# Optimization experiments

Hardware: AMD Instinct MI355X
Metric: run time of the kernel (lower is better)

The kernel has to match this reference:

```python
import jax, jax.numpy as jnp
import numpy as np

EPS = 1e-5
K = 3
K2 = K * K


def _conv(x, w, pad=0):
    return jax.lax.conv_general_dilated(
        x, w, (1, 1), [(pad, pad), (pad, pad)],
        dimension_numbers=('NCHW', 'OIHW', 'NCHW'))


def _bn_silu(x, gamma, beta, mean, var):
    scale = (gamma / jnp.sqrt(var + EPS))[None, :, None, None]
    y = (x - mean[None, :, None, None]) * scale + beta[None, :, None, None]
    return y * jax.nn.sigmoid(y)  # SiLU


def _space_to_depth(x, s=2):
    b, c, h, w = x.shape
    x = x.reshape(b, c, h // s, s, w // s, s)
    x = x.transpose(0, 1, 3, 5, 2, 4)
    return x.reshape(b, c * s * s, h // s, w // s)


def _deform_sample(x, offset, mask, pad=1):
    # x: (B,C,H,W); offset: (B,2*K2,H,W) layout [kk -> (dy,dx)]; mask: (B,K2,H,W)
    B, C, H, W = x.shape
    off = offset.reshape(B, K2, 2, H, W)
    oy, ox = off[:, :, 0], off[:, :, 1]
    ki = jnp.repeat(jnp.arange(K), K)  # kernel row (y), (K2,)
    kj = jnp.tile(jnp.arange(K), K)    # kernel col (x), (K2,)
    base_y = (jnp.arange(H)[None, :, None] - pad + ki[:, None, None]).astype(x.dtype)  # (K2,H,1)
    base_x = (jnp.arange(W)[None, None, :] - pad + kj[:, None, None]).astype(x.dtype)  # (K2,1,W)
    py = base_y[None] + oy  # (B,K2,H,W)
    px = base_x[None] + ox

    y0 = jnp.floor(py)
    x0 = jnp.floor(px)
    wy = py - y0
    wx = px - x0
    y0i = y0.astype(jnp.int32)
    x0i = x0.astype(jnp.int32)

    xf = x.reshape(B, C, H * W)
    gather = jax.vmap(lambda a, i: a[:, i])  # (C,HW),(N)->(C,N)

    out = jnp.zeros((B, C, K2, H, W), x.dtype)
    for dy in (0, 1):
        for dx in (0, 1):
            yi = y0i + dy
            xi = x0i + dx
            valid = (yi >= 0) & (yi < H) & (xi >= 0) & (xi < W)
            w = (wy if dy else 1.0 - wy) * (wx if dx else 1.0 - wx) * valid
            idx = (jnp.clip(yi, 0, H - 1) * W + jnp.clip(xi, 0, W - 1)).reshape(B, -1)
            vals = gather(xf, idx).reshape(B, C, K2, H, W)
            out = out + vals * w[:, None]
    return out * mask[:, None]  # modulated


def setup_inputs() -> dict:
    key = jax.random.key(0)
    ks = jax.random.split(key, 12)
    B, C1, H, W = 8, 128, 160, 160
    C_SPD, C_MID, C2 = C1 * 4, 128, 256
    inp = {
        'x': jax.random.normal(ks[0], (B, C1, H, W), jnp.float32),
        'reduce_w': jax.random.normal(ks[1], (C_MID, C_SPD, 1, 1), jnp.float32) * 0.05,
        'reduce_gamma': jax.random.uniform(ks[2], (C_MID,), jnp.float32, 0.5, 1.5),
        'reduce_beta': jax.random.normal(ks[3], (C_MID,), jnp.float32) * 0.1,
        'reduce_mean': jax.random.normal(ks[4], (C_MID,), jnp.float32) * 0.1,
        'reduce_var': jax.random.uniform(ks[5], (C_MID,), jnp.float32, 0.5, 1.5),
        'off_w': jax.random.normal(ks[6], (27, C_MID, 3, 3), jnp.float32) * 0.01,
        'off_b': jnp.zeros((27,), jnp.float32),
        'dcn_w': jax.random.normal(ks[7], (C2, C_MID, 3, 3), jnp.float32) * 0.03,
        'dcn_gamma': jax.random.uniform(ks[8], (C2,), jnp.float32, 0.5, 1.5),
        'dcn_beta': jax.random.normal(ks[9], (C2,), jnp.float32) * 0.1,
        'dcn_mean': jax.random.normal(ks[10], (C2,), jnp.float32) * 0.1,
        'dcn_var': jax.random.uniform(ks[11], (C2,), jnp.float32, 0.5, 1.5),
    }
    return inp


def reference(x, reduce_w, reduce_gamma, reduce_beta, reduce_mean, reduce_var,
              off_w, off_b, dcn_w, dcn_gamma, dcn_beta, dcn_mean, dcn_var):
    # SPD: (B,C,H,W) -> (B,4C,H/2,W/2)
    x = _space_to_depth(x, 2)
    # 1x1 reduce + BN + SiLU
    x = _bn_silu(_conv(x, reduce_w), reduce_gamma, reduce_beta, reduce_mean, reduce_var)
    # offset/mask prediction (3x3 conv, pad=1)
    om = _conv(x, off_w, pad=1) + off_b[None, :, None, None]
    offset = om[:, :2 * K2]
    mask = jax.nn.sigmoid(om[:, 2 * K2:3 * K2])
    # modulated deformable 3x3 conv (stride 1, pad 1)
    samp = _deform_sample(x, offset, mask, pad=1)  # (B,C_mid,9,H,W)
    O = dcn_w.shape[0]
    out = jnp.einsum('bckhw,ock->bohw', samp, dcn_w.reshape(O, dcn_w.shape[1], K2))
    return _bn_silu(out, dcn_gamma, dcn_beta, dcn_mean, dcn_var)
```

## Files before the change

### kernel.cpp

```cpp
#include <hip/hip_runtime.h>

constexpr int HW  = 6400;
constexpr int WW  = 80;

typedef __attribute__((ext_vector_type(8))) short short8;
typedef __attribute__((ext_vector_type(4))) float f32x4;
typedef unsigned short ushort_t;

__device__ __forceinline__ float sigmoidf_(float x) { return 1.f / (1.f + __expf(-x)); }
__device__ __forceinline__ float siluf_(float y) { return y / (1.f + __expf(-y)); }
__device__ __forceinline__ ushort_t f2bf(float f) {
    unsigned u = __float_as_uint(f);
    u += 0x7FFFu + ((u >> 16) & 1u);
    return (ushort_t)(u >> 16);
}
__device__ __forceinline__ float bf2f(ushort_t h) {
    return __uint_as_float(((unsigned)h) << 16);
}
__device__ __forceinline__ int xcd_bid800(int b) { return (b & 7) * 100 + (b >> 3); }

__global__ __launch_bounds__(256) void k0_prep(
    const float* __restrict__ rw, const float* __restrict__ ow,
    const float* __restrict__ dw,
    const float* __restrict__ rg, const float* __restrict__ rb,
    const float* __restrict__ rm, const float* __restrict__ rv,
    ushort_t* __restrict__ WB,
    ushort_t* __restrict__ WoB, ushort_t* __restrict__ WdB,
    float* __restrict__ scr, float* __restrict__ shr)
{
    const int i = blockIdx.x * 256 + threadIdx.x;
    if (blockIdx.x == 0 && threadIdx.x < 128) {
        const int m = threadIdx.x;
        const float sc = rg[m] * rsqrtf(rv[m] + 1e-5f);
        scr[m] = sc;
        shr[m] = rb[m] - rm[m] * sc;
    }
    if (i < 65536) {
        const int e = i & 7;
        const int lane = (i >> 3) & 63;
        const int chunkW = i >> 9;
        const int nt = chunkW >> 4, kks = chunkW & 15;
        const int kk = kks * 32 + ((lane >> 4) << 3) + e;
        const int o = (nt << 4) + (lane & 15);
        WB[i] = f2bf(rw[o * 512 + kk]);
    }
    const int j = i - 65536;
    if (j >= 0 && j < 36864) {
        const int e = j & 7;
        const int lane = (j >> 3) & 63;
        const int chunk = j >> 9;
        const int nf = chunk / 36, ksg = chunk % 36;
        const int kk = ksg * 32 + ((lane >> 4) << 3) + e;
        const int q = kk >> 7, c = kk & 127;
        const int o = (nf << 4) + (lane & 15);
        WoB[j] = (o < 27) ? f2bf(ow[o * 1152 + c * 9 + q]) : (ushort_t)0;
    }
    const int l = j - 36864;
    if (l >= 0 && l < 294912) {
        const int e = l & 7;
        const int lane = (l >> 3) & 63;
        const int chunk = l >> 9;
        const int ot = chunk / 36, ksg = chunk % 36;
        const int kk = ksg * 32 + ((lane >> 4) << 3) + e;
        const int tap = kk >> 7, c = kk & 127;
        const int o = (ot << 4) + (lane & 15);
        WdB[l] = f2bf(dw[o * 1152 + c * 9 + tap]);
    }
}

__global__ __launch_bounds__(256) void k1_reduce(
    const float* __restrict__ x,
    const ushort_t* __restrict__ WB,
    const float* __restrict__ scr, const float* __restrict__ shr,
    ushort_t* __restrict__ xm_bf)
{
    const int t    = threadIdx.x;
    const int lane = t & 63;
    const int wave = t >> 6;
    const int q = lane >> 4, ln = lane & 15;
    const int p0 = xcd_bid800(blockIdx.x) * 64;
    const int bb = p0 / HW;
    const int px = wave * 16 + ln;
    const int hw = (p0 % HW) + px;
    const int h = hw / WW, w = hw % WW;
    const float* xb = x + (size_t)bb * 128 * 25600 + (2 * h) * 160 + 2 * w;

    f32x4 acc[8] = {};

#pragma unroll 4
    for (int kks = 0; kks < 16; ++kks) {
        const int c0 = kks * 8 + q * 2;
        const float* pc0 = xb + (size_t)c0 * 25600;
        const float* pc1 = pc0 + 25600;
        const float2 a0 = *reinterpret_cast<const float2*>(pc0);
        const float2 a1 = *reinterpret_cast<const float2*>(pc0 + 160);
        const float2 b0 = *reinterpret_cast<const float2*>(pc1);
        const float2 b1 = *reinterpret_cast<const float2*>(pc1 + 160);
        short8 p;
        p[0] = (short)f2bf(a0.x); p[1] = (short)f2bf(a0.y);
        p[2] = (short)f2bf(a1.x); p[3] = (short)f2bf(a1.y);
        p[4] = (short)f2bf(b0.x); p[5] = (short)f2bf(b0.y);
        p[6] = (short)f2bf(b1.x); p[7] = (short)f2bf(b1.y);
#pragma unroll
        for (int nt = 0; nt < 8; ++nt) {
            const short8 wf = *reinterpret_cast<const short8*>(WB + ((nt << 4) + kks) * 512 + lane * 8);
            acc[nt] = __builtin_amdgcn_mfma_f32_16x16x32_bf16(wf, p, acc[nt], 0, 0, 0);
        }
    }

    const int pi = p0 + px;
    ushort_t* op = xm_bf + (size_t)pi * 128;
#pragma unroll
    for (int nt = 0; nt < 8; ++nt) {
        const int ob = nt * 16 + q * 4;
        const float4 s4 = *reinterpret_cast<const float4*>(scr + ob);
        const float4 b4 = *reinterpret_cast<const float4*>(shr + ob);
        const float y0 = siluf_(acc[nt][0] * s4.x + b4.x);
        const float y1 = siluf_(acc[nt][1] * s4.y + b4.y);
        const float y2 = siluf_(acc[nt][2] * s4.z + b4.z);
        const float y3 = siluf_(acc[nt][3] * s4.w + b4.w);
        *reinterpret_cast<uint2*>(op + ob) =
            make_uint2(f2bf(y0) | ((unsigned)f2bf(y1) << 16),
                       f2bf(y2) | ((unsigned)f2bf(y3) << 16));
    }
}

__global__ __launch_bounds__(256) void k2_off(
    const ushort_t* __restrict__ xm_bf, const ushort_t* __restrict__ WoB,
    const float* __restrict__ obias, float* __restrict__ om)
{
    __shared__ __align__(16) ushort_t A[2][64 * 128];
    __shared__ __align__(16) float T[32 * 64];

    const int t = threadIdx.x;
    const int lane = t & 63;
    const int wave = t >> 6;
    const int p0 = xcd_bid800(blockIdx.x) * 64;
    const int bb = p0 / HW;
    const int hw0 = p0 % HW;

    const int spx = t & 63;
    const int hws = hw0 + spx;
    const int hh = hws / WW, wwp = hws % WW;

    auto STAGE = [&](int q, int buf) {
        const int dy = q / 3 - 1, dx = q % 3 - 1;
        const int y = hh + dy, xx = wwp + dx;
        const bool valid = ((unsigned)y < 80u) && ((unsigned)xx < 80u);
        const ushort_t* src = xm_bf + ((size_t)bb * HW + y * WW + xx) * 128 + wave * 32;
#pragma unroll
        for (int s = 0; s < 4; ++s) {
            uint4 v = make_uint4(0u, 0u, 0u, 0u);
            if (valid) v = *reinterpret_cast<const uint4*>(src + s * 8);
            const int cslot = wave * 4 + s;
            *reinterpret_cast<uint4*>(&A[buf][spx * 128 + ((cslot ^ (spx & 7)) << 3)]) = v;
        }
    };

    const int q4 = lane >> 4, ln = lane & 15;
    f32x4 acc[2] = {};

    auto GEMM = [&](int q, int buf) {
#pragma unroll
        for (int ks = 0; ks < 4; ++ks) {
            const int px = wave * 16 + ln;
            const int elem = px * 128 + (((ks * 4 + q4) ^ (px & 7)) << 3);
            const short8 a = *reinterpret_cast<const short8*>(&A[buf][elem]);
#pragma unroll
            for (int nf = 0; nf < 2; ++nf) {
                const int chunk = nf * 36 + q * 4 + ks;
                const short8 b = *reinterpret_cast<const short8*>(WoB + chunk * 512 + lane * 8);
                acc[nf] = __builtin_amdgcn_mfma_f32_16x16x32_bf16(a, b, acc[nf], 0, 0, 0);
            }
        }
    };

    STAGE(0, 0);
    __syncthreads();
    for (int q = 0; q < 9; ++q) {
        if (q < 8) STAGE(q + 1, (q + 1) & 1);
        GEMM(q, q & 1);
        __syncthreads();
    }

#pragma unroll
    for (int nf = 0; nf < 2; ++nf)
#pragma unroll
        for (int r = 0; r < 4; ++r) {
            const int o = nf * 16 + ln;
            const int px = wave * 16 + q4 * 4 + r;
            T[o * 64 + px] = acc[nf][r];
        }
    __syncthreads();
    for (int i = t; i < 27 * 64; i += 256) {
        const int o = i >> 6, px = i & 63;
        om[((size_t)bb * 27 + o) * HW + hw0 + px] = T[i] + obias[o];
    }
}

__global__ __launch_bounds__(512) void k3_dcn(
    const ushort_t* __restrict__ xm_bf, const float* __restrict__ om,
    const ushort_t* __restrict__ WdB,
    const float* __restrict__ g, const float* __restrict__ be,
    const float* __restrict__ mu, const float* __restrict__ va,
    float* __restrict__ out)
{
    __shared__ __align__(16) ushort_t S[2][64 * 128];
    __shared__ __align__(16) float4 geoW[9][64];
    __shared__ __align__(16) int4   geoI[9][64];

    const int t    = threadIdx.x;
    const int lane = t & 63;
    const int wave = t >> 6;
    const int p0   = xcd_bid800(blockIdx.x) * 64;
    const int bb   = p0 / HW;
    const int hw0  = p0 % HW;

    for (int it = t; it < 576; it += 512) {
        const int tap = it >> 6, px = it & 63;
        const int hw = hw0 + px;
        const int h = hw / WW, w = hw % WW;
        const float* ob = om + (size_t)bb * 27 * HW + hw;
        const float oy = ob[(2 * tap) * HW];
        const float ox = ob[(2 * tap + 1) * HW];
        const float mk = sigmoidf_(ob[(18 + tap) * HW]);
        float py  = (float)(h - 1 + tap / 3) + oy;
        float pxf = (float)(w - 1 + tap % 3) + ox;
        py  = fminf(fmaxf(py, -1000.f), 1000.f);
        pxf = fminf(fmaxf(pxf, -1000.f), 1000.f);
        const float fy = floorf(py), fx = floorf(pxf);
        const int y0 = (int)fy, x0 = (int)fx, y1 = y0 + 1, x1 = x0 + 1;
        const float wy = py - fy, wx = pxf - fx;
        const float vy0 = ((unsigned)y0 < 80u) ? 1.f : 0.f;
        const float vy1 = ((unsigned)y1 < 80u) ? 1.f : 0.f;
        const float vx0 = ((unsigned)x0 < 80u) ? 1.f : 0.f;
        const float vx1 = ((unsigned)x1 < 80u) ? 1.f : 0.f;
        float4 wv;
        wv.x = (1.f - wy) * (1.f - wx) * vy0 * vx0 * mk;
        wv.y = (1.f - wy) * wx * vy0 * vx1 * mk;
        wv.z = wy * (1.f - wx) * vy1 * vx0 * mk;
        wv.w = wy * wx * vy1 * vx1 * mk;
        const int cy0 = min(max(y0, 0), 79), cy1 = min(max(y1, 0), 79);
        const int cx0 = min(max(x0, 0), 79), cx1 = min(max(x1, 0), 79);
        int4 iv;
        iv.x = cy0 * WW + cx0; iv.y = cy0 * WW + cx1;
        iv.z = cy1 * WW + cx0; iv.w = cy1 * WW + cx1;
        geoW[tap][px] = wv;
        geoI[tap][px] = iv;
    }
    __syncthreads();

    const ushort_t* xb = xm_bf + (size_t)bb * HW * 128;

    const int spx = t >> 3;
    const int scg = t & 7;

    uint4 pr[8];

    auto ISSUE = [&](int tap) {
        const int4 iv = geoI[tap][spx];
        const uint4* c00 = reinterpret_cast<const uint4*>(xb + (size_t)iv.x * 128 + scg * 16);
        const uint4* c01 = reinterpret_cast<const uint4*>(xb + (size_t)iv.y * 128 + scg * 16);
        const uint4* c10 = reinterpret_cast<const uint4*>(xb + (size_t)iv.z * 128 + scg * 16);
        const uint4* c11 = reinterpret_cast<const uint4*>(xb + (size_t)iv.w * 128 + scg * 16);
        pr[0] = c00[0]; pr[1] = c00[1];
        pr[2] = c01[0]; pr[3] = c01[1];
        pr[4] = c10[0]; pr[5] = c10[1];
        pr[6] = c11[0]; pr[7] = c11[1];
    };

    auto BLEND_WRITE = [&](int tap, int bufIdx) {
        const float4 wv = geoW[tap][spx];
#pragma unroll
        for (int half = 0; half < 2; ++half) {
            const unsigned* ap = (const unsigned*)&pr[0 + half];
            const unsigned* bp = (const unsigned*)&pr[2 + half];
            const unsigned* cp = (const unsigned*)&pr[4 + half];
            const unsigned* dp = (const unsigned*)&pr[6 + half];
            unsigned pk[4];
#pragma unroll
            for (int u = 0; u < 4; ++u) {
                const float alo = __uint_as_float(ap[u] << 16), ahi = __uint_as_float(ap[u] & 0xFFFF0000u);
                const float blo = __uint_as_float(bp[u] << 16), bhi = __uint_as_float(bp[u] & 0xFFFF0000u);
                const float clo = __uint_as_float(cp[u] << 16), chi = __uint_as_float(cp[u] & 0xFFFF0000u);
                const float dlo = __uint_as_float(dp[u] << 16), dhi = __uint_as_float(dp[u] & 0xFFFF0000u);
                const float slo = wv.x * alo + wv.y * blo + wv.z * clo + wv.w * dlo;
                const float shi = wv.x * ahi + wv.y * bhi + wv.z * chi + wv.w * dhi;
                pk[u] = (unsigned)f2bf(slo) | ((unsigned)f2bf(shi) << 16);
            }
            const int cslot = scg * 2 + half;
            const int elem  = spx * 128 + ((cslot ^ (spx & 7)) << 3);
            *reinterpret_cast<uint4*>(&S[bufIdx][elem]) =
                make_uint4(pk[0], pk[1], pk[2], pk[3]);
        }
    };

    const int wM = wave >> 2, wN = wave & 3;
    const int q = lane >> 4, ln = lane & 15;
    f32x4 acc[2][4] = {};

    auto GEMM = [&](int tap, int bufIdx) {
#pragma unroll
        for (int ks = 0; ks < 4; ++ks) {
            short8 a0, a1;
            {
                const int px = wM * 32 + ln;
                const int elem = px * 128 + (((ks * 4 + q) ^ (px & 7)) << 3);
                a0 = *reinterpret_cast<const short8*>(&S[bufIdx][elem]);
            }
            {
                const int px = wM * 32 + 16 + ln;
                const int elem = px * 128 + (((ks * 4 + q) ^ (px & 7)) << 3);
                a1 = *reinterpret_cast<const short8*>(&S[bufIdx][elem]);
            }
#pragma unroll
            for (int nt = 0; nt < 4; ++nt) {
                const int ot = wN * 4 + nt;
                const int chunk = ot * 36 + tap * 4 + ks;
                const short8 b = *reinterpret_cast<const short8*>(WdB + chunk * 512 + lane * 8);
                acc[0][nt] = __builtin_amdgcn_mfma_f32_16x16x32_bf16(a0, b, acc[0][nt], 0, 0, 0);
                acc[1][nt] = __builtin_amdgcn_mfma_f32_16x16x32_bf16(a1, b, acc[1][nt], 0, 0, 0);
            }
        }
    };

    ISSUE(0);
    BLEND_WRITE(0, 0);
    __syncthreads();

    for (int tap = 0; tap < 9; ++tap) {
        if (tap < 8) ISSUE(tap + 1);
        GEMM(tap, tap & 1);
        if (tap < 8) BLEND_WRITE(tap + 1, (tap + 1) & 1);
        __syncthreads();
    }

    float sc[4], sh[4];
#pragma unroll
    for (int nt = 0; nt < 4; ++nt) {
        const int o = wN * 64 + nt * 16 + ln;
        sc[nt] = g[o] * rsqrtf(va[o] + 1e-5f);
        sh[nt] = be[o] - mu[o] * sc[nt];
    }
#pragma unroll
    for (int mt = 0; mt < 2; ++mt)
#pragma unroll
        for (int nt = 0; nt < 4; ++nt) {
            const int o = wN * 64 + nt * 16 + ln;
            float* obase = out + (size_t)bb * 256 * HW + (size_t)o * HW;
            float4 st;
            st.x = siluf_(acc[mt][nt][0] * sc[nt] + sh[nt]);
            st.y = siluf_(acc[mt][nt][1] * sc[nt] + sh[nt]);
            st.z = siluf_(acc[mt][nt][2] * sc[nt] + sh[nt]);
            st.w = siluf_(acc[mt][nt][3] * sc[nt] + sh[nt]);
            *reinterpret_cast<float4*>(obase + hw0 + wM * 32 + mt * 16 + q * 4) = st;
        }
}

extern "C" void kernel_launch(void* const* d_in, const int* in_sizes, int n_in,
                              void* d_out, int out_size, void* d_ws, size_t ws_size,
                              hipStream_t stream)
{
    const float* x        = (const float*)d_in[0];
    const float* reduce_w = (const float*)d_in[1];
    const float* rg       = (const float*)d_in[2];
    const float* rb       = (const float*)d_in[3];
    const float* rm       = (const float*)d_in[4];
    const float* rv       = (const float*)d_in[5];
    const float* off_w    = (const float*)d_in[6];
    const float* off_b    = (const float*)d_in[7];
    const float* dcn_w    = (const float*)d_in[8];
    const float* dg       = (const float*)d_in[9];
    const float* db       = (const float*)d_in[10];
    const float* dm       = (const float*)d_in[11];
    const float* dv       = (const float*)d_in[12];

    float* ws  = (float*)d_ws;
    ushort_t* xm_bf = (ushort_t*)ws;
    float* om   = ws + 3276800;
    ushort_t* WB   = (ushort_t*)(om + 1382400);
    ushort_t* WoB  = WB + 65536;
    ushort_t* WdB  = WoB + 36864;
    float* scr = (float*)(WdB + 294912);
    float* shr = scr + 128;

    k0_prep<<<dim3(1552), dim3(256), 0, stream>>>(reduce_w, off_w, dcn_w,
                                                  rg, rb, rm, rv,
                                                  WB, WoB, WdB, scr, shr);
    k1_reduce<<<dim3(800), dim3(256), 0, stream>>>(x, WB, scr, shr, xm_bf);
    k2_off<<<dim3(800), dim3(256), 0, stream>>>(xm_bf, WoB, off_b, om);
    k3_dcn<<<dim3(800), dim3(512), 0, stream>>>(xm_bf, om, WdB, dg, db, dm, dv, (float*)d_out);
}
```

Before: 167.0 us.

## Fuse offset/mask 3x3 conv into deformable conv kernel

Removes the separate offset-prediction kernel and computes the 27-channel 3x3 conv inside the DCN kernel per 64-pixel tile, keeping the results in shared memory instead of writing and re-reading an fp32 offset/mask tensor in global memory. The offset-conv work is now split across 8 waves, one 16x16 MFMA tile each, with shared memory reused between the conv tile, its transpose buffer and the geometry tables. This saves a kernel launch and the om round trip. In exchange the DCN kernel takes on extra prologue work and synchronisation, and may use more registers or shared memory, which could lower occupancy.

```diff
diff --git a/kernel.cpp b/kernel.cpp
--- a/kernel.cpp
+++ b/kernel.cpp
@@ -125,89 +125,19 @@
     }
 }
 
-__global__ __launch_bounds__(256) void k2_off(
-    const ushort_t* __restrict__ xm_bf, const ushort_t* __restrict__ WoB,
-    const float* __restrict__ obias, float* __restrict__ om)
-{
-    __shared__ __align__(16) ushort_t A[2][64 * 128];
-    __shared__ __align__(16) float T[32 * 64];
-
-    const int t = threadIdx.x;
-    const int lane = t & 63;
-    const int wave = t >> 6;
-    const int p0 = xcd_bid800(blockIdx.x) * 64;
-    const int bb = p0 / HW;
-    const int hw0 = p0 % HW;
-
-    const int spx = t & 63;
-    const int hws = hw0 + spx;
-    const int hh = hws / WW, wwp = hws % WW;
-
-    auto STAGE = [&](int q, int buf) {
-        const int dy = q / 3 - 1, dx = q % 3 - 1;
-        const int y = hh + dy, xx = wwp + dx;
-        const bool valid = ((unsigned)y < 80u) && ((unsigned)xx < 80u);
-        const ushort_t* src = xm_bf + ((size_t)bb * HW + y * WW + xx) * 128 + wave * 32;
-#pragma unroll
-        for (int s = 0; s < 4; ++s) {
-            uint4 v = make_uint4(0u, 0u, 0u, 0u);
-            if (valid) v = *reinterpret_cast<const uint4*>(src + s * 8);
-            const int cslot = wave * 4 + s;
-            *reinterpret_cast<uint4*>(&A[buf][spx * 128 + ((cslot ^ (spx & 7)) << 3)]) = v;
-        }
-    };
-
-    const int q4 = lane >> 4, ln = lane & 15;
-    f32x4 acc[2] = {};
-
-    auto GEMM = [&](int q, int buf) {
-#pragma unroll
-        for (int ks = 0; ks < 4; ++ks) {
-            const int px = wave * 16 + ln;
-            const int elem = px * 128 + (((ks * 4 + q4) ^ (px & 7)) << 3);
-            const short8 a = *reinterpret_cast<const short8*>(&A[buf][elem]);
-#pragma unroll
-            for (int nf = 0; nf < 2; ++nf) {
-                const int chunk = nf * 36 + q * 4 + ks;
-                const short8 b = *reinterpret_cast<const short8*>(WoB + chunk * 512 + lane * 8);
-                acc[nf] = __builtin_amdgcn_mfma_f32_16x16x32_bf16(a, b, acc[nf], 0, 0, 0);
-            }
-        }
-    };
-
-    STAGE(0, 0);
-    __syncthreads();
-    for (int q = 0; q < 9; ++q) {
-        if (q < 8) STAGE(q + 1, (q + 1) & 1);
-        GEMM(q, q & 1);
-        __syncthreads();
-    }
-
-#pragma unroll
-    for (int nf = 0; nf < 2; ++nf)
-#pragma unroll
-        for (int r = 0; r < 4; ++r) {
-            const int o = nf * 16 + ln;
-            const int px = wave * 16 + q4 * 4 + r;
-            T[o * 64 + px] = acc[nf][r];
-        }
-    __syncthreads();
-    for (int i = t; i < 27 * 64; i += 256) {
-        const int o = i >> 6, px = i & 63;
-        om[((size_t)bb * 27 + o) * HW + hw0 + px] = T[i] + obias[o];
-    }
-}
-
 __global__ __launch_bounds__(512) void k3_dcn(
-    const ushort_t* __restrict__ xm_bf, const float* __restrict__ om,
+    const ushort_t* __restrict__ xm_bf,
+    const ushort_t* __restrict__ WoB, const float* __restrict__ obias,
     const ushort_t* __restrict__ WdB,
     const float* __restrict__ g, const float* __restrict__ be,
     const float* __restrict__ mu, const float* __restrict__ va,
     float* __restrict__ out)
 {
-    __shared__ __align__(16) ushort_t S[2][64 * 128];
-    __shared__ __align__(16) float4 geoW[9][64];
-    __shared__ __align__(16) int4   geoI[9][64];
+    __shared__ __align__(16) ushort_t AS[2][64 * 128];
+    __shared__ __align__(16) char R1[18432];
+    float*  T    = (float*)R1;
+    float4* geoWf = (float4*)R1;
+    int4*   geoIf = (int4*)(R1 + 9216);
 
     const int t    = threadIdx.x;
     const int lane = t & 63;
@@ -215,50 +145,115 @@
     const int p0   = xcd_bid800(blockIdx.x) * 64;
     const int bb   = p0 / HW;
     const int hw0  = p0 % HW;
-
-    for (int it = t; it < 576; it += 512) {
-        const int tap = it >> 6, px = it & 63;
-        const int hw = hw0 + px;
-        const int h = hw / WW, w = hw % WW;
-        const float* ob = om + (size_t)bb * 27 * HW + hw;
-        const float oy = ob[(2 * tap) * HW];
-        const float ox = ob[(2 * tap + 1) * HW];
-        const float mk = sigmoidf_(ob[(18 + tap) * HW]);
-        float py  = (float)(h - 1 + tap / 3) + oy;
-        float pxf = (float)(w - 1 + tap % 3) + ox;
-        py  = fminf(fmaxf(py, -1000.f), 1000.f);
-        pxf = fminf(fmaxf(pxf, -1000.f), 1000.f);
-        const float fy = floorf(py), fx = floorf(pxf);
-        const int y0 = (int)fy, x0 = (int)fx, y1 = y0 + 1, x1 = x0 + 1;
-        const float wy = py - fy, wx = pxf - fx;
-        const float vy0 = ((unsigned)y0 < 80u) ? 1.f : 0.f;
-        const float vy1 = ((unsigned)y1 < 80u) ? 1.f : 0.f;
-        const float vx0 = ((unsigned)x0 < 80u) ? 1.f : 0.f;
-        const float vx1 = ((unsigned)x1 < 80u) ? 1.f : 0.f;
-        float4 wv;
-        wv.x = (1.f - wy) * (1.f - wx) * vy0 * vx0 * mk;
-        wv.y = (1.f - wy) * wx * vy0 * vx1 * mk;
-        wv.z = wy * (1.f - wx) * vy1 * vx0 * mk;
-        wv.w = wy * wx * vy1 * vx1 * mk;
-        const int cy0 = min(max(y0, 0), 79), cy1 = min(max(y1, 0), 79);
-        const int cx0 = min(max(x0, 0), 79), cx1 = min(max(x1, 0), 79);
-        int4 iv;
-        iv.x = cy0 * WW + cx0; iv.y = cy0 * WW + cx1;
-        iv.z = cy1 * WW + cx0; iv.w = cy1 * WW + cx1;
-        geoW[tap][px] = wv;
-        geoI[tap][px] = iv;
-    }
-    __syncthreads();
+    const int q = lane >> 4, ln = lane & 15;
 
     const ushort_t* xb = xm_bf + (size_t)bb * HW * 128;
+
+    {
+        const int spx = t & 63;
+        const int hws = hw0 + spx;
+        const int hh = hws / WW, wwp = hws % WW;
+        const int mt2 = wave & 3;
+        const int nf2 = wave >> 2;
+
+        auto STAGE2 = [&](int qq, int buf) {
+            const int dy = qq / 3 - 1, dx = qq % 3 - 1;
+            const int y = hh + dy, xx = wwp + dx;
+            const bool valid = ((unsigned)y < 80u) && ((unsigned)xx < 80u);
+            const ushort_t* src = xb + ((size_t)(y * WW + xx)) * 128 + wave * 16;
+#pragma unroll
+            for (int s = 0; s < 2; ++s) {
+                uint4 v = make_uint4(0u, 0u, 0u, 0u);
+                if (valid) v = *reinterpret_cast<const uint4*>(src + s * 8);
+                const int cslot = wave * 2 + s;
+                *reinterpret_cast<uint4*>(&AS[buf][spx * 128 + ((cslot ^ (spx & 7)) << 3)]) = v;
+            }
+        };
+
+        f32x4 acc2 = {};
+        auto GEMM2 = [&](int qq, int buf) {
+#pragma unroll
+            for (int ks = 0; ks < 4; ++ks) {
+                const int px = mt2 * 16 + ln;
+                const int elem = px * 128 + (((ks * 4 + q) ^ (px & 7)) << 3);
+                const short8 a = *reinterpret_cast<const short8*>(&AS[buf][elem]);
+                const int chunk = nf2 * 36 + qq * 4 + ks;
+                const short8 b = *reinterpret_cast<const short8*>(WoB + chunk * 512 + lane * 8);
+                acc2 = __builtin_amdgcn_mfma_f32_16x16x32_bf16(a, b, acc2, 0, 0, 0);
+            }
+        };
+
+        STAGE2(0, 0);
+        __syncthreads();
+        for (int qq = 0; qq < 9; ++qq) {
+            if (qq < 8) STAGE2(qq + 1, (qq + 1) & 1);
+            GEMM2(qq, qq & 1);
+            __syncthreads();
+        }
+#pragma unroll
+        for (int r = 0; r < 4; ++r) {
+            const int o = nf2 * 16 + ln;
+            const int px = mt2 * 16 + q * 4 + r;
+            T[o * 64 + px] = acc2[r];
+        }
+        __syncthreads();
+    }
+
+    {
+        float goy[2], gox[2], gmk[2];
+#pragma unroll
+        for (int k2i = 0; k2i < 2; ++k2i) {
+            const int it = t + k2i * 512;
+            if (it < 576) {
+                const int tap = it >> 6, px = it & 63;
+                goy[k2i] = T[(2 * tap) * 64 + px] + obias[2 * tap];
+                gox[k2i] = T[(2 * tap + 1) * 64 + px] + obias[2 * tap + 1];
+                gmk[k2i] = sigmoidf_(T[(18 + tap) * 64 + px] + obias[18 + tap]);
+            }
+        }
+        __syncthreads();
+#pragma unroll
+        for (int k2i = 0; k2i < 2; ++k2i) {
+            const int it = t + k2i * 512;
+            if (it < 576) {
+                const int tap = it >> 6, px = it & 63;
+                const int hw = hw0 + px;
+                const int h = hw / WW, w = hw % WW;
+                float py  = (float)(h - 1 + tap / 3) + goy[k2i];
+                float pxf = (float)(w - 1 + tap % 3) + gox[k2i];
+                py  = fminf(fmaxf(py, -1000.f), 1000.f);
+                pxf = fminf(fmaxf(pxf, -1000.f), 1000.f);
+                const float fy = floorf(py), fx = floorf(pxf);
+                const int y0 = (int)fy, x0 = (int)fx, y1 = y0 + 1, x1 = x0 + 1;
+                const float wy = py - fy, wx = pxf - fx;
+                const float vy0 = ((unsigned)y0 < 80u) ? 1.f : 0.f;
+                const float vy1 = ((unsigned)y1 < 80u) ? 1.f : 0.f;
+                const float vx0 = ((unsigned)x0 < 80u) ? 1.f : 0.f;
+                const float vx1 = ((unsigned)x1 < 80u) ? 1.f : 0.f;
+                float4 wv;
+                const float mk = gmk[k2i];
+                wv.x = (1.f - wy) * (1.f - wx) * vy0 * vx0 * mk;
+                wv.y = (1.f - wy) * wx * vy0 * vx1 * mk;
+                wv.z = wy * (1.f - wx) * vy1 * vx0 * mk;
+                wv.w = wy * wx * vy1 * vx1 * mk;
+                const int cy0 = min(max(y0, 0), 79), cy1 = min(max(y1, 0), 79);
+                const int cx0 = min(max(x0, 0), 79), cx1 = min(max(x1, 0), 79);
+                int4 iv;
+                iv.x = cy0 * WW + cx0; iv.y = cy0 * WW + cx1;
+                iv.z = cy1 * WW + cx0; iv.w = cy1 * WW + cx1;
+                geoWf[tap * 64 + px] = wv;
+                geoIf[tap * 64 + px] = iv;
+            }
+        }
+        __syncthreads();
+    }
 
     const int spx = t >> 3;
     const int scg = t & 7;
-
     uint4 pr[8];
 
     auto ISSUE = [&](int tap) {
-        const int4 iv = geoI[tap][spx];
+        const int4 iv = geoIf[tap * 64 + spx];
         const uint4* c00 = reinterpret_cast<const uint4*>(xb + (size_t)iv.x * 128 + scg * 16);
         const uint4* c01 = reinterpret_cast<const uint4*>(xb + (size_t)iv.y * 128 + scg * 16);
         const uint4* c10 = reinterpret_cast<const uint4*>(xb + (size_t)iv.z * 128 + scg * 16);
@@ -270,7 +265,7 @@
     };
 
     auto BLEND_WRITE = [&](int tap, int bufIdx) {
-        const float4 wv = geoW[tap][spx];
+        const float4 wv = geoWf[tap * 64 + spx];
 #pragma unroll
         for (int half = 0; half < 2; ++half) {
             const unsigned* ap = (const unsigned*)&pr[0 + half];
@@ -290,13 +285,12 @@
             }
             const int cslot = scg * 2 + half;
             const int elem  = spx * 128 + ((cslot ^ (spx & 7)) << 3);
-            *reinterpret_cast<uint4*>(&S[bufIdx][elem]) =
+            *reinterpret_cast<uint4*>(&AS[bufIdx][elem]) =
                 make_uint4(pk[0], pk[1], pk[2], pk[3]);
         }
     };
 
     const int wM = wave >> 2, wN = wave & 3;
-    const int q = lane >> 4, ln = lane & 15;
     f32x4 acc[2][4] = {};
 
     auto GEMM = [&](int tap, int bufIdx) {
@@ -306,12 +300,12 @@
             {
                 const int px = wM * 32 + ln;
                 const int elem = px * 128 + (((ks * 4 + q) ^ (px & 7)) << 3);
-                a0 = *reinterpret_cast<const short8*>(&S[bufIdx][elem]);
+                a0 = *reinterpret_cast<const short8*>(&AS[bufIdx][elem]);
             }
             {
                 const int px = wM * 32 + 16 + ln;
                 const int elem = px * 128 + (((ks * 4 + q) ^ (px & 7)) << 3);
-                a1 = *reinterpret_cast<const short8*>(&S[bufIdx][elem]);
+                a1 = *reinterpret_cast<const short8*>(&AS[bufIdx][elem]);
             }
 #pragma unroll
             for (int nt = 0; nt < 4; ++nt) {
@@ -388,6 +382,6 @@
                                                   rg, rb, rm, rv,
                                                   WB, WoB, WdB, scr, shr);
     k1_reduce<<<dim3(800), dim3(256), 0, stream>>>(x, WB, scr, shr, xm_bf);
-    k2_off<<<dim3(800), dim3(256), 0, stream>>>(xm_bf, WoB, off_b, om);
-    k3_dcn<<<dim3(800), dim3(512), 0, stream>>>(xm_bf, om, WdB, dg, db, dm, dv, (float*)d_out);
-}
+    k3_dcn<<<dim3(800), dim3(512), 0, stream>>>(xm_bf, WoB, off_b, WdB,
+                                                dg, db, dm, dv, (float*)d_out);
+}
```

New measurement: 158.5 us. -5.1%, faster.
